# Kernel tuning notes

Measured on AMD Instinct MI355X. Metric: run time of the kernel, lower is better.

The kernel has to match this reference:

```python
import jax, jax.numpy as jnp
import numpy as np

D_MODEL = 1024
NUM_HEADS = 16
D_FF = 4096
EPS = 1e-5


def _linear(x, w, b):
    # torch nn.Linear: y = x @ W^T + b, W is [out, in]
    return jnp.einsum('bld,od->blo', x, w) + b


def _layer_norm(x, g, b):
    mu = jnp.mean(x, axis=-1, keepdims=True)
    var = jnp.mean(jnp.square(x - mu), axis=-1, keepdims=True)
    return (x - mu) / jnp.sqrt(var + EPS) * g + b


def _mha(q, k, v, wq, bq, wk, bk, wv, bv, wo, bo, mask, num_heads):
    B, Lq, D = q.shape
    hd = D // num_heads
    Q = _linear(q, wq, bq).reshape(B, Lq, num_heads, hd).transpose(0, 2, 1, 3)
    K = _linear(k, wk, bk).reshape(B, -1, num_heads, hd).transpose(0, 2, 1, 3)
    V = _linear(v, wv, bv).reshape(B, -1, num_heads, hd).transpose(0, 2, 1, 3)
    scale = jnp.sqrt(jnp.asarray(hd, dtype=q.dtype))
    energy = jnp.einsum('bhqd,bhkd->bhqk', Q, K) / scale  # [B,H,Lq,Lk]
    energy = jnp.where(mask, energy, jnp.asarray(-1e10, dtype=q.dtype))
    attn = jax.nn.softmax(energy, axis=-1)
    x = jnp.einsum('bhqk,bhkd->bhqd', attn, V)
    x = x.transpose(0, 2, 1, 3).reshape(B, Lq, D)
    return _linear(x, wo, bo), attn


def setup_inputs() -> dict:
    key = jax.random.key(0)
    ks = iter(jax.random.split(key, 40))
    B, T, S, D, F = 4, 1024, 1024, D_MODEL, D_FF
    inp = {
        'tgt': jax.random.normal(next(ks), (B, T, D), dtype=jnp.float32),
        'enc_src': jax.random.normal(next(ks), (B, S, D), dtype=jnp.float32),
        'tgt_mask': jnp.tril(jnp.ones((1, 1, T, T), dtype=bool)),
        'src_mask': jnp.ones((1, 1, 1, S), dtype=bool),
    }
    def lin(kk, o, i):
        return jax.random.normal(kk, (o, i), dtype=jnp.float32) * 0.02
    for pfx in ('sa', 'ca'):  # self-attn and cross-attn params
        for nm in ('q', 'k', 'v', 'o'):
            inp[f'{pfx}_w{nm}'] = lin(next(ks), D, D)
            inp[f'{pfx}_b{nm}'] = jnp.zeros((D,), dtype=jnp.float32)
    inp['ff_w1'] = lin(next(ks), F, D)
    inp['ff_b1'] = jnp.zeros((F,), dtype=jnp.float32)
    inp['ff_w2'] = lin(next(ks), D, F)
    inp['ff_b2'] = jnp.zeros((D,), dtype=jnp.float32)
    for i in (1, 2, 3):
        inp[f'ln{i}_g'] = jnp.ones((D,), dtype=jnp.float32)
        inp[f'ln{i}_b'] = jnp.zeros((D,), dtype=jnp.float32)
    return inp


def reference(tgt, enc_src, tgt_mask, src_mask,
              sa_wq, sa_bq, sa_wk, sa_bk, sa_wv, sa_bv, sa_wo, sa_bo,
              ca_wq, ca_bq, ca_wk, ca_bk, ca_wv, ca_bv, ca_wo, ca_bo,
              ff_w1, ff_b1, ff_w2, ff_b2,
              ln1_g, ln1_b, ln2_g, ln2_b, ln3_g, ln3_b):
    # dropout in eval mode (identity)
    _t, _ = _mha(tgt, tgt, tgt, sa_wq, sa_bq, sa_wk, sa_bk, sa_wv, sa_bv,
                 sa_wo, sa_bo, tgt_mask, NUM_HEADS)
    tgt = _layer_norm(tgt + _t, ln1_g, ln1_b)
    _t, attention = _mha(tgt, enc_src, enc_src, ca_wq, ca_bq, ca_wk, ca_bk,
                         ca_wv, ca_bv, ca_wo, ca_bo, src_mask, NUM_HEADS)
    tgt = _layer_norm(tgt + _t, ln2_g, ln2_b)
    _t = _linear(jax.nn.relu(_linear(tgt, ff_w1, ff_b1)), ff_w2, ff_b2)
    tgt = _layer_norm(tgt + _t, ln3_g, ln3_b)
    return tgt, attention
```

## Files before the change

### kernel.cpp

```cpp
#include <hip/hip_runtime.h>
#include <hip/hip_bf16.h>

#define BBATCH 4
#define TT 1024
#define SS 1024
#define DD 1024
#define HH 16
#define HD 64
#define FFD 4096
#define MM (BBATCH*TT)

using f32x4  = __attribute__((ext_vector_type(4))) float;
using s16x8  = __attribute__((ext_vector_type(8))) short;
using bf16x8 = __attribute__((ext_vector_type(8))) __bf16;

__device__ __forceinline__ unsigned short f2b(float f) {
  union { float f; unsigned int u; } x{f};
  unsigned int r = x.u + 0x7FFFu + ((x.u >> 16) & 1u);
  return (unsigned short)(r >> 16);
}

__device__ __forceinline__ float b2f(unsigned short u) {
  union { unsigned int i; float f; } x; x.i = (unsigned int)u << 16; return x.f;
}

__device__ __forceinline__ void gload16(const void* g, void* l) {
  __builtin_amdgcn_global_load_lds(
      (const __attribute__((address_space(1))) void*)g,
      (__attribute__((address_space(3))) void*)l, 16, 0, 0);
}

__device__ __forceinline__ f32x4 mfma_bf16(s16x8 a, s16x8 b, f32x4 c) {
  return __builtin_amdgcn_mfma_f32_16x16x32_bf16(
      __builtin_bit_cast(bf16x8, a), __builtin_bit_cast(bf16x8, b), c, 0, 0, 0);
}

__device__ __forceinline__ void xcd_swz(int gx, int& bn, int& bm) {
  int flat = blockIdx.y * gx + blockIdx.x;
  int nwg = gx * gridDim.y;
  int swz = (flat & 7) * (nwg >> 3) + (flat >> 3);
  bn = swz % gx; bm = swz / gx;
}

template <int JT>
__device__ __forceinline__ void stage_ab(
    const unsigned short* __restrict__ Ab, int lda,
    const unsigned short* __restrict__ Bb, int ldb,
    int kk, unsigned short* As, unsigned short* Bs, int r0, int c0, int wave)
{
#pragma unroll
  for (int s = 0; s < 2; s++) {
    int k2 = kk + s * 32;
    gload16(Ab + (size_t)r0 * lda + k2 + c0, As + s * 4096 + wave * 512);
    gload16(Ab + (size_t)(r0 + 64) * lda + k2 + c0, As + s * 4096 + wave * 512 + 2048);
    gload16(Bb + (size_t)r0 * ldb + k2 + c0, Bs + s * (JT * 1024) + wave * 512);
    if (JT == 4)
      gload16(Bb + (size_t)(r0 + 64) * ldb + k2 + c0, Bs + s * (JT * 1024) + wave * 512 + 2048);
  }
}

template <int JT>
__device__ __forceinline__ void gemm_core_db(
    const unsigned short* __restrict__ Ab, int lda,
    const unsigned short* __restrict__ Bb, int ldb,
    int K, unsigned short* As, unsigned short* Bs, f32x4 (&acc)[4][JT])
{
  const int tid = threadIdx.x, wave = tid >> 6, lane = tid & 63;
  const int r0 = tid >> 2, c0 = (tid & 3) * 8;
  const int wrow = (wave >> 1) * 64, wcol = (wave & 1) * 16 * JT;
  const int q = lane >> 4, rl = lane & 15;

  stage_ab<JT>(Ab, lda, Bb, ldb, 0, As, Bs, r0, c0, wave);
  const int nt = K >> 6;
  for (int t = 0; t < nt; t++) {
    __syncthreads();
    if (t + 1 < nt)
      stage_ab<JT>(Ab, lda, Bb, ldb, (t + 1) << 6,
                   As + ((t + 1) & 1) * 8192, Bs + ((t + 1) & 1) * (JT * 2048),
                   r0, c0, wave);
    const s16x8* Av = (const s16x8*)(As + (t & 1) * 8192);
    const s16x8* Bv = (const s16x8*)(Bs + (t & 1) * (JT * 2048));
#pragma unroll
    for (int s = 0; s < 2; s++) {
      s16x8 af[4], bfr[JT];
#pragma unroll
      for (int u = 0; u < 4; u++) af[u] = Av[s * 512 + (wrow + u * 16 + rl) * 4 + q];
#pragma unroll
      for (int u = 0; u < JT; u++) bfr[u] = Bv[s * (JT * 128) + (wcol + u * 16 + rl) * 4 + q];
#pragma unroll
      for (int i = 0; i < 4; i++)
#pragma unroll
        for (int j = 0; j < JT; j++)
          acc[i][j] = mfma_bf16(af[i], bfr[j], acc[i][j]);
    }
  }
}

template <int EPI, int JT>
__global__ __launch_bounds__(256) void gemm_bt(
    const unsigned short* __restrict__ A, int lda,
    const unsigned short* __restrict__ B, int ldb,
    const float* __restrict__ bias, const float* __restrict__ res,
    float* __restrict__ Cf, unsigned short* __restrict__ Cb, int ldc, int K)
{
  __shared__ __align__(16) unsigned short As[2 * 8192];
  __shared__ __align__(16) unsigned short Bs[2 * JT * 2048];
  int bm, bn;
  xcd_swz(gridDim.x, bn, bm);
  const int lane = threadIdx.x & 63, wave = threadIdx.x >> 6;
  const int wrow = (wave >> 1) * 64, wcol = (wave & 1) * 16 * JT;
  const int q = lane >> 4, rl = lane & 15;

  f32x4 acc[4][JT];
  f32x4 z = {0.f, 0.f, 0.f, 0.f};
#pragma unroll
  for (int i = 0; i < 4; i++)
#pragma unroll
    for (int j = 0; j < JT; j++) acc[i][j] = z;

  gemm_core_db<JT>(A + (size_t)bm * 128 * lda, lda,
                   B + (size_t)bn * (32 * JT) * ldb, ldb, K, As, Bs, acc);

#pragma unroll
  for (int i = 0; i < 4; i++) {
    int gm0 = bm * 128 + wrow + i * 16 + q * 4;
#pragma unroll
    for (int j = 0; j < JT; j++) {
      int gn = bn * (32 * JT) + wcol + j * 16 + rl;
      float bv = bias[gn];
#pragma unroll
      for (int r = 0; r < 4; r++) {
        size_t off = (size_t)(gm0 + r) * ldc + gn;
        float v = acc[i][j][r];
        if constexpr (EPI == 0) Cb[off] = f2b(v + bv);
        else if constexpr (EPI == 2) Cf[off] = v + bv + res[off];
        else Cb[off] = f2b(fmaxf(v + bv, 0.f));
      }
    }
  }
}

__global__ __launch_bounds__(256) void gemm_qkvkv(
    const unsigned short* __restrict__ Xb, const unsigned short* __restrict__ Eb,
    const unsigned short* __restrict__ Wqkv1, const unsigned short* __restrict__ Wkv2,
    const float* __restrict__ bqkv, const float* __restrict__ bkv,
    unsigned short* __restrict__ QKVb, unsigned short* __restrict__ KVb,
    unsigned short* __restrict__ Vt1, unsigned short* __restrict__ Vt2)
{
  __shared__ __align__(16) unsigned short lds[32768];
  unsigned short* As = lds;
  unsigned short* Bs = lds + 16384;
  const int tid = threadIdx.x;
  int bm, bn;
  xcd_swz(gridDim.x, bn, bm);
  const int lane = tid & 63, wave = tid >> 6;
  const int wrow = (wave >> 1) * 64, wcol = (wave & 1) * 64;
  const int q = lane >> 4, rl = lane & 15;

  const unsigned short *A, *Bw;
  const float* bias;
  unsigned short *C, *Vt;
  int ldc, vbn;
  bool isV;
  if (bn < 24) {
    A = Xb; Bw = Wqkv1 + (size_t)bn * 128 * 1024; bias = bqkv + bn * 128;
    C = QKVb + bn * 128; ldc = 3072;
    isV = (bn >= 16); Vt = Vt1; vbn = bn - 16;
  } else {
    int b2 = bn - 24;
    A = Eb; Bw = Wkv2 + (size_t)b2 * 128 * 1024; bias = bkv + b2 * 128;
    C = KVb + b2 * 128; ldc = 2048;
    isV = (b2 >= 8); Vt = Vt2; vbn = b2 - 8;
  }

  f32x4 acc[4][4];
  f32x4 z = {0.f, 0.f, 0.f, 0.f};
#pragma unroll
  for (int i = 0; i < 4; i++)
#pragma unroll
    for (int j = 0; j < 4; j++) acc[i][j] = z;

  gemm_core_db<4>(A + (size_t)bm * 128 * 1024, 1024, Bw, 1024, 1024, As, Bs, acc);

  if (!isV) {
#pragma unroll
    for (int i = 0; i < 4; i++) {
      int lr0 = wrow + i * 16 + q * 4;
#pragma unroll
      for (int j = 0; j < 4; j++) {
        int lc = wcol + j * 16 + rl;
        float bv = bias[lc];
#pragma unroll
        for (int r = 0; r < 4; r++)
          C[(size_t)(bm * 128 + lr0 + r) * ldc + lc] = f2b(acc[i][j][r] + bv);
      }
    }
  } else {
    __syncthreads();
#pragma unroll
    for (int i = 0; i < 4; i++) {
      int lr0 = wrow + i * 16 + q * 4;
#pragma unroll
      for (int j = 0; j < 4; j++) {
        int lc = wcol + j * 16 + rl;
        float bv = bias[lc];
        int base = lc * 128, sw = (lc & 7) << 2;
#pragma unroll
        for (int r = 0; r < 4; r++)
          lds[base + ((lr0 + r) ^ sw)] = f2b(acc[i][j][r] + bv);
      }
    }
    __syncthreads();
    const int b = bm >> 3, s0 = (bm & 7) * 128;
#pragma unroll
    for (int it = 0; it < 16; it++) {
      int idx = it * 256 + tid;
      int lc = idx >> 5, qa = idx & 31;
      ushort4 v4 = *(const ushort4*)&lds[lc * 128 + ((qa ^ (lc & 7)) << 2)];
      int h = vbn * 2 + (lc >> 6), d = lc & 63;
      *(ushort4*)&Vt[(((size_t)b * 16 + h) * 64 + d) * 1024 + s0 + qa * 4] = v4;
    }
  }
}

__device__ __forceinline__ void stage_k(
    const unsigned short* src, int ldk, unsigned short* Kbuf,
    int r0, int c0, int wave)
{
#pragma unroll
  for (int kq = 0; kq < 2; kq++) {
    gload16(src + (size_t)r0 * ldk + kq * 32 + c0, Kbuf + kq * 4096 + wave * 512);
    gload16(src + (size_t)(r0 + 64) * ldk + kq * 32 + c0, Kbuf + kq * 4096 + wave * 512 + 2048);
  }
}

__device__ __forceinline__ void sblock_qk(
    const unsigned short* Qs, const unsigned short* Ks,
    int wrow, int wcol, int q, int rl, f32x4 (&acc)[4][4])
{
  const s16x8* Qv = (const s16x8*)Qs;
  const s16x8* Kv = (const s16x8*)Ks;
  f32x4 z = {0.f, 0.f, 0.f, 0.f};
#pragma unroll
  for (int i = 0; i < 4; i++)
#pragma unroll
    for (int j = 0; j < 4; j++) acc[i][j] = z;
#pragma unroll
  for (int kq = 0; kq < 2; kq++) {
    s16x8 af[4], bf[4];
#pragma unroll
    for (int t = 0; t < 4; t++) af[t] = Qv[kq * 512 + (wrow + t * 16 + rl) * 4 + q];
#pragma unroll
    for (int t = 0; t < 4; t++) bf[t] = Kv[kq * 512 + (wcol + t * 16 + rl) * 4 + q];
#pragma unroll
    for (int i = 0; i < 4; i++)
#pragma unroll
      for (int j = 0; j < 4; j++)
        acc[i][j] = mfma_bf16(af[i], bf[j], acc[i][j]);
  }
}

__device__ __forceinline__ void load_vf(
    const unsigned short* Vbase, int c, int wc2, int q, int rl, s16x8 (&vf)[4][2])
{
#pragma unroll
  for (int ks = 0; ks < 4; ks++)
#pragma unroll
    for (int t = 0; t < 2; t++)
      vf[ks][t] = *(const s16x8*)(Vbase + (size_t)(wc2 + t * 16 + rl) * SS +
                                  c * 128 + ks * 32 + q * 8);
}

__device__ __forceinline__ void store_ps_swz(
    unsigned short* Ps, const f32x4 (&acc)[4][4], int wrow, int wcol, int q, int rl)
{
#pragma unroll
  for (int i = 0; i < 4; i++)
#pragma unroll
    for (int j = 0; j < 4; j++) {
      int col = wcol + j * 16 + rl;
      int ks = col >> 5, cc = col & 31;
#pragma unroll
      for (int r = 0; r < 4; r++) {
        int row = wrow + i * 16 + q * 4 + r;
        int unit = (row * 4 + (cc >> 3)) ^ ((row >> 1) & 3);
        Ps[ks * 4096 + unit * 8 + (cc & 7)] = f2b(acc[i][j][r]);
      }
    }
}

__device__ __forceinline__ void pv_swz(
    const unsigned short* Ps, const s16x8 (&vf)[4][2],
    int wrow, int q, int rl, f32x4 (&oacc)[4][2])
{
  const s16x8* Pv = (const s16x8*)Ps;
#pragma unroll
  for (int ks = 0; ks < 4; ks++) {
    s16x8 af[4];
#pragma unroll
    for (int t = 0; t < 4; t++) {
      int row = wrow + t * 16 + rl;
      af[t] = Pv[ks * 512 + ((row * 4 + q) ^ ((row >> 1) & 3))];
    }
#pragma unroll
    for (int i = 0; i < 4; i++)
#pragma unroll
      for (int jt = 0; jt < 2; jt++)
        oacc[i][jt] = mfma_bf16(af[i], vf[ks][jt], oacc[i][jt]);
  }
}

__global__ __launch_bounds__(256, 2) void flash_sa(
    const unsigned short* __restrict__ Qg, int ldq,
    const unsigned short* __restrict__ Kg, int ldk,
    const unsigned short* __restrict__ Vt,
    unsigned short* __restrict__ Og)
{
  __shared__ __align__(16) unsigned short Qs[2 * 128 * 32];
  __shared__ __align__(16) unsigned short Ks[2][2 * 128 * 32];
  __shared__ __align__(16) unsigned short Ps[4 * 128 * 32];

  const int tid = threadIdx.x, wave = tid >> 6, lane = tid & 63;
  const int q = lane >> 4, rl = lane & 15;
  const int bh = blockIdx.y, b = bh >> 4, h = bh & 15;
  const int bm = (bh & 32) ? (7 - blockIdx.x) : blockIdx.x;
  const int wrow = (wave >> 1) * 64, wcol = (wave & 1) * 64;
  const int wc2 = (wave & 1) * 32;
  const int r0 = tid >> 2, c0 = (tid & 3) * 8;

  const unsigned short* Qbase = Qg + ((size_t)b * TT + bm * 128) * ldq + h * HD;
  const unsigned short* Kbase = Kg + (size_t)b * SS * ldk + h * HD;
  const unsigned short* Vbase = Vt + ((size_t)bh << 16);

#pragma unroll
  for (int kq = 0; kq < 2; kq++) {
    gload16(Qbase + (size_t)r0 * ldq + kq * 32 + c0, Qs + kq * 4096 + wave * 512);
    gload16(Qbase + (size_t)(r0 + 64) * ldq + kq * 32 + c0, Qs + kq * 4096 + wave * 512 + 2048);
  }
  stage_k(Kbase, ldk, Ks[0], r0, c0, wave);
  const int nch = bm + 1;

  float l_run[4][4];
  f32x4 oacc[4][2];
  f32x4 z = {0.f, 0.f, 0.f, 0.f};
#pragma unroll
  for (int i = 0; i < 4; i++) {
    oacc[i][0] = z; oacc[i][1] = z;
#pragma unroll
    for (int r = 0; r < 4; r++) l_run[i][r] = 0.f;
  }

  for (int c = 0; c < nch; c++) {
    __syncthreads();
    if (c + 1 < nch)
      stage_k(Kbase + (size_t)(c + 1) * 128 * ldk, ldk, Ks[(c + 1) & 1], r0, c0, wave);
    s16x8 vf[4][2];
    load_vf(Vbase, c, wc2, q, rl, vf);
    f32x4 acc[4][4];
    sblock_qk(Qs, Ks[c & 1], wrow, wcol, q, rl, acc);
#pragma unroll
    for (int i = 0; i < 4; i++)
#pragma unroll
      for (int r = 0; r < 4; r++) {
#pragma unroll
        for (int j = 0; j < 4; j++) {
          float v = acc[i][j][r] * 0.125f;
          bool msk = (c == bm) && (wcol + j * 16 + rl) > (wrow + i * 16 + q * 4 + r);
          acc[i][j][r] = msk ? 0.f : __expf(v);
        }
        float s = acc[i][0][r] + acc[i][1][r] + acc[i][2][r] + acc[i][3][r];
#pragma unroll
        for (int off = 1; off < 16; off <<= 1) s += __shfl_xor(s, off);
        l_run[i][r] += s;
      }
    store_ps_swz(Ps, acc, wrow, wcol, q, rl);
    __syncthreads();
    pv_swz(Ps, vf, wrow, q, rl, oacc);
  }
  __syncthreads();

  float* red = (float*)Ps;
  if (rl == 0) {
#pragma unroll
    for (int i = 0; i < 4; i++)
#pragma unroll
      for (int r = 0; r < 4; r++)
        red[(wave & 1) * 128 + wrow + i * 16 + q * 4 + r] = l_run[i][r];
  }
  __syncthreads();

#pragma unroll
  for (int i = 0; i < 4; i++) {
#pragma unroll
    for (int r = 0; r < 4; r++) {
      int row = wrow + i * 16 + q * 4 + r;
      float inv = 1.0f / (red[row] + red[128 + row]);
      int grow = bm * 128 + row;
#pragma unroll
      for (int jt = 0; jt < 2; jt++) {
        int col = h * HD + wc2 + jt * 16 + rl;
        Og[((size_t)b * TT + grow) * DD + col] = f2b(oacc[i][jt][r] * inv);
      }
    }
  }
}

__global__ __launch_bounds__(256, 2) void flash_ca(
    const unsigned short* __restrict__ Qg, int ldq,
    const unsigned short* __restrict__ Kg, int ldk,
    const unsigned short* __restrict__ Vt,
    float* __restrict__ Pout,
    unsigned short* __restrict__ Og)
{
  __shared__ __align__(16) unsigned short Qs[2 * 128 * 32];
  __shared__ __align__(16) unsigned short Ks[2][2 * 128 * 32];
  __shared__ __align__(16) unsigned short Ps[4 * 128 * 32];

  const int tid = threadIdx.x, wave = tid >> 6, lane = tid & 63;
  const int q = lane >> 4, rl = lane & 15;
  const int bm = blockIdx.x, bh = blockIdx.y, b = bh >> 4, h = bh & 15;
  const int wrow = (wave >> 1) * 64, wcol = (wave & 1) * 64;
  const int wc2 = (wave & 1) * 32;
  const int r0 = tid >> 2, c0 = (tid & 3) * 8;

  const unsigned short* Qbase = Qg + ((size_t)b * TT + bm * 128) * ldq + h * HD;
  const unsigned short* Kbase = Kg + (size_t)b * SS * ldk + h * HD;
  const unsigned short* Vbase = Vt + ((size_t)bh << 16);

#pragma unroll
  for (int kq = 0; kq < 2; kq++) {
    gload16(Qbase + (size_t)r0 * ldq + kq * 32 + c0, Qs + kq * 4096 + wave * 512);
    gload16(Qbase + (size_t)(r0 + 64) * ldq + kq * 32 + c0, Qs + kq * 4096 + wave * 512 + 2048);
  }
  stage_k(Kbase, ldk, Ks[0], r0, c0, wave);

  float l_run[4][4];
#pragma unroll
  for (int i = 0; i < 4; i++)
#pragma unroll
    for (int r = 0; r < 4; r++) l_run[i][r] = 0.f;

  for (int c = 0; c < 8; c++) {
    __syncthreads();
    if (c < 7)
      stage_k(Kbase + (size_t)(c + 1) * 128 * ldk, ldk, Ks[(c + 1) & 1], r0, c0, wave);
    f32x4 acc[4][4];
    sblock_qk(Qs, Ks[c & 1], wrow, wcol, q, rl, acc);
#pragma unroll
    for (int i = 0; i < 4; i++)
#pragma unroll
      for (int r = 0; r < 4; r++) {
        float s = __expf(acc[i][0][r] * 0.125f) + __expf(acc[i][1][r] * 0.125f) +
                  __expf(acc[i][2][r] * 0.125f) + __expf(acc[i][3][r] * 0.125f);
#pragma unroll
        for (int off = 1; off < 16; off <<= 1) s += __shfl_xor(s, off);
        l_run[i][r] += s;
      }
  }
  float* red = (float*)Ps;
  if (rl == 0) {
#pragma unroll
    for (int i = 0; i < 4; i++)
#pragma unroll
      for (int r = 0; r < 4; r++)
        red[(wave & 1) * 128 + wrow + i * 16 + q * 4 + r] = l_run[i][r];
  }
  __syncthreads();
  float invl[4][4];
#pragma unroll
  for (int i = 0; i < 4; i++)
#pragma unroll
    for (int r = 0; r < 4; r++) {
      int row = wrow + i * 16 + q * 4 + r;
      invl[i][r] = 1.0f / (red[row] + red[128 + row]);
    }

  f32x4 oacc[4][2];
  f32x4 z = {0.f, 0.f, 0.f, 0.f};
#pragma unroll
  for (int i = 0; i < 4; i++) { oacc[i][0] = z; oacc[i][1] = z; }
  stage_k(Kbase, ldk, Ks[0], r0, c0, wave);

  for (int c = 0; c < 8; c++) {
    __syncthreads();
    if (c < 7)
      stage_k(Kbase + (size_t)(c + 1) * 128 * ldk, ldk, Ks[(c + 1) & 1], r0, c0, wave);
    s16x8 vf[4][2];
    load_vf(Vbase, c, wc2, q, rl, vf);
    f32x4 acc[4][4];
    sblock_qk(Qs, Ks[c & 1], wrow, wcol, q, rl, acc);
#pragma unroll
    for (int i = 0; i < 4; i++)
#pragma unroll
      for (int j = 0; j < 4; j++)
#pragma unroll
        for (int r = 0; r < 4; r++)
          acc[i][j][r] = __expf(acc[i][j][r] * 0.125f) * invl[i][r];
    store_ps_swz(Ps, acc, wrow, wcol, q, rl);
    __syncthreads();
#pragma unroll
    for (int it = 0; it < 8; it++) {
      int idx = it * 256 + tid;
      int ks = idx >> 9, rw = (idx >> 2) & 127, u = idx & 3;
      s16x8 pv = ((const s16x8*)Ps)[ks * 512 + ((rw * 4 + u) ^ ((rw >> 1) & 3))];
      float4 lo = make_float4(b2f((unsigned short)pv[0]), b2f((unsigned short)pv[1]),
                              b2f((unsigned short)pv[2]), b2f((unsigned short)pv[3]));
      float4 hi = make_float4(b2f((unsigned short)pv[4]), b2f((unsigned short)pv[5]),
                              b2f((unsigned short)pv[6]), b2f((unsigned short)pv[7]));
      float* dst = Pout + ((size_t)bh << 20) + ((size_t)(bm * 128 + rw) << 10) +
                   c * 128 + ks * 32 + u * 8;
      ((float4*)dst)[0] = lo;
      ((float4*)dst)[1] = hi;
    }
    pv_swz(Ps, vf, wrow, q, rl, oacc);
  }

#pragma unroll
  for (int i = 0; i < 4; i++)
#pragma unroll
    for (int jt = 0; jt < 2; jt++)
#pragma unroll
      for (int r = 0; r < 4; r++) {
        int row = bm * 128 + wrow + i * 16 + q * 4 + r;
        int col = h * HD + wc2 + jt * 16 + rl;
        Og[((size_t)b * TT + row) * DD + col] = f2b(oacc[i][jt][r]);
      }
}

__global__ __launch_bounds__(256) void ln_k(
    const float* __restrict__ src, const float* __restrict__ g,
    const float* __restrict__ b, float* __restrict__ dstf,
    unsigned short* __restrict__ dstb)
{
  __shared__ float sh[10];
  const size_t row = blockIdx.x;
  const int tid = threadIdx.x;
  float4 v = ((const float4*)(src + (row << 10)))[tid];
  float s = v.x + v.y + v.z + v.w;
  float ss = v.x * v.x + v.y * v.y + v.z * v.z + v.w * v.w;
  for (int o = 32; o; o >>= 1) { s += __shfl_down(s, o); ss += __shfl_down(ss, o); }
  if ((tid & 63) == 0) { sh[tid >> 6] = s; sh[4 + (tid >> 6)] = ss; }
  __syncthreads();
  if (tid == 0) {
    sh[8] = sh[0] + sh[1] + sh[2] + sh[3];
    sh[9] = sh[4] + sh[5] + sh[6] + sh[7];
  }
  __syncthreads();
  const float mean = sh[8] * (1.0f / DD);
  const float var = sh[9] * (1.0f / DD) - mean * mean;
  const float inv = rsqrtf(var + 1e-5f);
  float4 gv = ((const float4*)g)[tid];
  float4 bv = ((const float4*)b)[tid];
  float4 y;
  y.x = (v.x - mean) * inv * gv.x + bv.x;
  y.y = (v.y - mean) * inv * gv.y + bv.y;
  y.z = (v.z - mean) * inv * gv.z + bv.z;
  y.w = (v.w - mean) * inv * gv.w + bv.w;
  if (dstf) ((float4*)(dstf + (row << 10)))[tid] = y;
  if (dstb) {
    ushort4 o = make_ushort4(f2b(y.x), f2b(y.y), f2b(y.z), f2b(y.w));
    ((ushort4*)(dstb + (row << 10)))[tid] = o;
  }
}

struct CvtArgs {
  const float* src[12];
  unsigned short* dst[12];
  const float *bq, *bk, *bv, *bk2, *bv2;
  float *bqkv, *bkv;
};

__global__ __launch_bounds__(256) void cvt_all(CvtArgs a) {
  const int blk = blockIdx.x;
  if (blk >= 24576) {
    int i = (blk - 24576) * 256 + threadIdx.x;
    if (i < 1024) a.bqkv[i] = a.bq[i];
    else if (i < 2048) a.bqkv[i] = a.bk[i - 1024];
    else if (i < 3072) a.bqkv[i] = a.bv[i - 2048];
    else if (i < 4096) a.bkv[i - 3072] = a.bk2[i - 3072];
    else if (i < 5120) a.bkv[i - 3072] = a.bv2[i - 4096 + 1024];
    return;
  }
  constexpr int st[13] = {0,       1048576, 2097152, 2359296, 2621440,
                          2883584, 3145728, 3407872, 3670016, 3932160,
                          4194304, 5242880, 6291456};
  int i = blk * 256 + threadIdx.x;
  int s = 0;
#pragma unroll
  for (int k = 1; k < 12; k++) s += (i >= st[k]) ? 1 : 0;
  int j = i - st[s];
  float4 v = ((const float4*)a.src[s])[j];
  ushort4 o = make_ushort4(f2b(v.x), f2b(v.y), f2b(v.z), f2b(v.w));
  ((ushort4*)a.dst[s])[j] = o;
}


extern "C" void kernel_launch(void* const* d_in, const int* in_sizes, int n_in,
                              void* d_out, int out_size, void* d_ws, size_t ws_size,
                              hipStream_t stream)
{
  const float* tgt = (const float*)d_in[0];
  const float* enc = (const float*)d_in[1];
  const float* sa_wq = (const float*)d_in[4];  const float* sa_bq = (const float*)d_in[5];
  const float* sa_wk = (const float*)d_in[6];  const float* sa_bk = (const float*)d_in[7];
  const float* sa_wv = (const float*)d_in[8];  const float* sa_bv = (const float*)d_in[9];
  const float* sa_wo = (const float*)d_in[10]; const float* sa_bo = (const float*)d_in[11];
  const float* ca_wq = (const float*)d_in[12]; const float* ca_bq = (const float*)d_in[13];
  const float* ca_wk = (const float*)d_in[14]; const float* ca_bk = (const float*)d_in[15];
  const float* ca_wv = (const float*)d_in[16]; const float* ca_bv = (const float*)d_in[17];
  const float* ca_wo = (const float*)d_in[18]; const float* ca_bo = (const float*)d_in[19];
  const float* ff_w1 = (const float*)d_in[20]; const float* ff_b1 = (const float*)d_in[21];
  const float* ff_w2 = (const float*)d_in[22]; const float* ff_b2 = (const float*)d_in[23];
  const float* ln1_g = (const float*)d_in[24]; const float* ln1_b = (const float*)d_in[25];
  const float* ln2_g = (const float*)d_in[26]; const float* ln2_b = (const float*)d_in[27];
  const float* ln3_g = (const float*)d_in[28]; const float* ln3_b = (const float*)d_in[29];

  float* out_tgt = (float*)d_out;
  float* out_attn = (float*)d_out + (size_t)MM * DD;

  char* w = (char*)d_ws;
  size_t off = 0;
  auto alloc = [&](size_t bytes) { void* p = w + off; off += (bytes + 255) & ~(size_t)255; return p; };
  unsigned short* Xb   = (unsigned short*)alloc((size_t)MM * DD * 2);
  unsigned short* Eb   = (unsigned short*)alloc((size_t)MM * DD * 2);
  unsigned short* Wq1  = (unsigned short*)alloc((size_t)DD * DD * 2);
  unsigned short* Wk1  = (unsigned short*)alloc((size_t)DD * DD * 2);
  unsigned short* Wv1  = (unsigned short*)alloc((size_t)DD * DD * 2);
  unsigned short* Wo1  = (unsigned short*)alloc((size_t)DD * DD * 2);
  unsigned short* Wq2  = (unsigned short*)alloc((size_t)DD * DD * 2);
  unsigned short* Wk2  = (unsigned short*)alloc((size_t)DD * DD * 2);
  unsigned short* Wv2  = (unsigned short*)alloc((size_t)DD * DD * 2);
  unsigned short* Wo2  = (unsigned short*)alloc((size_t)DD * DD * 2);
  unsigned short* Wf1  = (unsigned short*)alloc((size_t)FFD * DD * 2);
  unsigned short* Wf2  = (unsigned short*)alloc((size_t)DD * FFD * 2);
  unsigned short* QKVb = (unsigned short*)alloc((size_t)MM * 3 * DD * 2);
  unsigned short* KVb  = (unsigned short*)alloc((size_t)MM * 2 * DD * 2);
  unsigned short* Qca  = (unsigned short*)alloc((size_t)MM * DD * 2);
  unsigned short* Vt1  = (unsigned short*)alloc((size_t)MM * DD * 2);
  unsigned short* Vt2  = (unsigned short*)alloc((size_t)MM * DD * 2);
  unsigned short* Ob   = (unsigned short*)alloc((size_t)MM * DD * 2);
  float*          res1 = (float*)alloc((size_t)MM * DD * 4);
  unsigned short* t1b  = (unsigned short*)alloc((size_t)MM * DD * 2);
  float*          res2 = (float*)alloc((size_t)MM * DD * 4);
  unsigned short* t2b  = (unsigned short*)alloc((size_t)MM * DD * 2);
  unsigned short* Fb   = (unsigned short*)alloc((size_t)MM * FFD * 2);
  float*          bqkv = (float*)alloc(3072 * 4);
  float*          bkv  = (float*)alloc(2048 * 4);

  CvtArgs ca;
  ca.src[0] = tgt;   ca.dst[0] = Xb;
  ca.src[1] = enc;   ca.dst[1] = Eb;
  ca.src[2] = sa_wq; ca.dst[2] = Wq1;
  ca.src[3] = sa_wk; ca.dst[3] = Wk1;
  ca.src[4] = sa_wv; ca.dst[4] = Wv1;
  ca.src[5] = sa_wo; ca.dst[5] = Wo1;
  ca.src[6] = ca_wq; ca.dst[6] = Wq2;
  ca.src[7] = ca_wk; ca.dst[7] = Wk2;
  ca.src[8] = ca_wv; ca.dst[8] = Wv2;
  ca.src[9] = ca_wo; ca.dst[9] = Wo2;
  ca.src[10] = ff_w1; ca.dst[10] = Wf1;
  ca.src[11] = ff_w2; ca.dst[11] = Wf2;
  ca.bq = sa_bq; ca.bk = sa_bk; ca.bv = sa_bv; ca.bk2 = ca_bk; ca.bv2 = ca_bv;
  ca.bqkv = bqkv; ca.bkv = bkv;

  cvt_all<<<24596, 256, 0, stream>>>(ca);

  const dim3 gPRJ(40, 32);
  const dim3 gN64(16, 32);
  const dim3 gFF1(32, 32);
  const dim3 gFl(8, 64);

  gemm_qkvkv<<<gPRJ, 256, 0, stream>>>(Xb, Eb, Wq1, Wk2, bqkv, bkv,
                                       QKVb, KVb, Vt1, Vt2);

  flash_sa<<<gFl, 256, 0, stream>>>(QKVb, 3 * DD, QKVb + DD, 3 * DD, Vt1, Ob);
  gemm_bt<2, 2><<<gN64, 256, 0, stream>>>(Ob, DD, Wo1, DD, sa_bo, tgt, res1, nullptr, DD, DD);
  ln_k<<<MM, 256, 0, stream>>>(res1, ln1_g, ln1_b, res1, t1b);

  gemm_bt<0, 2><<<gN64, 256, 0, stream>>>(t1b, DD, Wq2, DD, ca_bq, nullptr, nullptr, Qca, DD, DD);
  flash_ca<<<gFl, 256, 0, stream>>>(Qca, DD, KVb, 2 * DD, Vt2, out_attn, Ob);
  gemm_bt<2, 2><<<gN64, 256, 0, stream>>>(Ob, DD, Wo2, DD, ca_bo, res1, res2, nullptr, DD, DD);
  ln_k<<<MM, 256, 0, stream>>>(res2, ln2_g, ln2_b, res2, t2b);

  gemm_bt<3, 4><<<gFF1, 256, 0, stream>>>(t2b, DD, Wf1, DD, ff_b1, nullptr, nullptr, Fb, FFD, DD);
  gemm_bt<2, 2><<<gN64, 256, 0, stream>>>(Fb, FFD, Wf2, FFD, ff_b2, res2, res1, nullptr, DD, FFD);
  ln_k<<<MM, 256, 0, stream>>>(res1, ln3_g, ln3_b, out_tgt, nullptr);
}
```

Baseline: 762.6 us.

## Load GEMM B operand directly into registers, bypassing LDS staging

The GEMM cores stop staging the weight (B) tile through shared memory. Each wave now loads its own B fragments straight from global memory into double-buffered registers one K-step ahead, and only A stays in LDS. This cuts LDS footprint and LDS read traffic, which may allow higher occupancy. In exchange it raises register pressure, and B rows are no longer shared between the two wave-rows, so the same B data is fetched twice from global/L2 with a less coalesced pattern.

```diff
diff --git a/kernel.cpp b/kernel.cpp
--- a/kernel.cpp
+++ b/kernel.cpp
@@ -42,57 +42,52 @@
   bn = swz % gx; bm = swz / gx;
 }
 
+__device__ __forceinline__ void stage_a(
+    const unsigned short* __restrict__ Ab, int lda, int kk,
+    unsigned short* As, int r0, int c0, int wave)
+{
+#pragma unroll
+  for (int s = 0; s < 2; s++) {
+    gload16(Ab + (size_t)r0 * lda + kk + s * 32 + c0, As + s * 4096 + wave * 512);
+    gload16(Ab + (size_t)(r0 + 64) * lda + kk + s * 32 + c0, As + s * 4096 + wave * 512 + 2048);
+  }
+}
+
 template <int JT>
-__device__ __forceinline__ void stage_ab(
+__device__ __forceinline__ void load_breg(
+    const unsigned short* __restrict__ Bl, int ldb, int kk, s16x8 (&br)[2][JT])
+{
+#pragma unroll
+  for (int s = 0; s < 2; s++)
+#pragma unroll
+    for (int u = 0; u < JT; u++)
+      br[s][u] = *(const s16x8*)(Bl + (size_t)u * 16 * ldb + kk + s * 32);
+}
+
+template <int JT>
+__device__ __forceinline__ void gemm_step(
     const unsigned short* __restrict__ Ab, int lda,
-    const unsigned short* __restrict__ Bb, int ldb,
-    int kk, unsigned short* As, unsigned short* Bs, int r0, int c0, int wave)
-{
+    const unsigned short* __restrict__ Bl, int ldb,
+    int t, int nt, unsigned short* AsCur, unsigned short* AsNext,
+    s16x8 (&brCur)[2][JT], s16x8 (&brNext)[2][JT],
+    f32x4 (&acc)[4][JT], int r0, int c0, int wave, int wrow, int q, int rl)
+{
+  __syncthreads();
+  if (t + 1 < nt) {
+    stage_a(Ab, lda, (t + 1) << 6, AsNext, r0, c0, wave);
+    load_breg<JT>(Bl, ldb, (t + 1) << 6, brNext);
+  }
+  const s16x8* Av = (const s16x8*)AsCur;
 #pragma unroll
   for (int s = 0; s < 2; s++) {
-    int k2 = kk + s * 32;
-    gload16(Ab + (size_t)r0 * lda + k2 + c0, As + s * 4096 + wave * 512);
-    gload16(Ab + (size_t)(r0 + 64) * lda + k2 + c0, As + s * 4096 + wave * 512 + 2048);
-    gload16(Bb + (size_t)r0 * ldb + k2 + c0, Bs + s * (JT * 1024) + wave * 512);
-    if (JT == 4)
-      gload16(Bb + (size_t)(r0 + 64) * ldb + k2 + c0, Bs + s * (JT * 1024) + wave * 512 + 2048);
-  }
-}
-
-template <int JT>
-__device__ __forceinline__ void gemm_core_db(
-    const unsigned short* __restrict__ Ab, int lda,
-    const unsigned short* __restrict__ Bb, int ldb,
-    int K, unsigned short* As, unsigned short* Bs, f32x4 (&acc)[4][JT])
-{
-  const int tid = threadIdx.x, wave = tid >> 6, lane = tid & 63;
-  const int r0 = tid >> 2, c0 = (tid & 3) * 8;
-  const int wrow = (wave >> 1) * 64, wcol = (wave & 1) * 16 * JT;
-  const int q = lane >> 4, rl = lane & 15;
-
-  stage_ab<JT>(Ab, lda, Bb, ldb, 0, As, Bs, r0, c0, wave);
-  const int nt = K >> 6;
-  for (int t = 0; t < nt; t++) {
-    __syncthreads();
-    if (t + 1 < nt)
-      stage_ab<JT>(Ab, lda, Bb, ldb, (t + 1) << 6,
-                   As + ((t + 1) & 1) * 8192, Bs + ((t + 1) & 1) * (JT * 2048),
-                   r0, c0, wave);
-    const s16x8* Av = (const s16x8*)(As + (t & 1) * 8192);
-    const s16x8* Bv = (const s16x8*)(Bs + (t & 1) * (JT * 2048));
-#pragma unroll
-    for (int s = 0; s < 2; s++) {
-      s16x8 af[4], bfr[JT];
-#pragma unroll
-      for (int u = 0; u < 4; u++) af[u] = Av[s * 512 + (wrow + u * 16 + rl) * 4 + q];
-#pragma unroll
-      for (int u = 0; u < JT; u++) bfr[u] = Bv[s * (JT * 128) + (wcol + u * 16 + rl) * 4 + q];
-#pragma unroll
-      for (int i = 0; i < 4; i++)
-#pragma unroll
-        for (int j = 0; j < JT; j++)
-          acc[i][j] = mfma_bf16(af[i], bfr[j], acc[i][j]);
-    }
+    s16x8 af[4];
+#pragma unroll
+    for (int u = 0; u < 4; u++) af[u] = Av[s * 512 + (wrow + u * 16 + rl) * 4 + q];
+#pragma unroll
+    for (int i = 0; i < 4; i++)
+#pragma unroll
+      for (int j = 0; j < JT; j++)
+        acc[i][j] = mfma_bf16(af[i], brCur[s][j], acc[i][j]);
   }
 }
 
@@ -104,12 +99,16 @@
     float* __restrict__ Cf, unsigned short* __restrict__ Cb, int ldc, int K)
 {
   __shared__ __align__(16) unsigned short As[2 * 8192];
-  __shared__ __align__(16) unsigned short Bs[2 * JT * 2048];
   int bm, bn;
   xcd_swz(gridDim.x, bn, bm);
-  const int lane = threadIdx.x & 63, wave = threadIdx.x >> 6;
+  const int tid = threadIdx.x;
+  const int lane = tid & 63, wave = tid >> 6;
   const int wrow = (wave >> 1) * 64, wcol = (wave & 1) * 16 * JT;
   const int q = lane >> 4, rl = lane & 15;
+  const int r0 = tid >> 2, c0 = (tid & 3) * 8;
+
+  const unsigned short* Ab = A + (size_t)bm * 128 * lda;
+  const unsigned short* Bl = B + (size_t)(bn * (32 * JT) + wcol + rl) * ldb + q * 8;
 
   f32x4 acc[4][JT];
   f32x4 z = {0.f, 0.f, 0.f, 0.f};
@@ -118,8 +117,16 @@
 #pragma unroll
     for (int j = 0; j < JT; j++) acc[i][j] = z;
 
-  gemm_core_db<JT>(A + (size_t)bm * 128 * lda, lda,
-                   B + (size_t)bn * (32 * JT) * ldb, ldb, K, As, Bs, acc);
+  s16x8 br0[2][JT], br1[2][JT];
+  stage_a(Ab, lda, 0, As, r0, c0, wave);
+  load_breg<JT>(Bl, ldb, 0, br0);
+  const int nt = K >> 6;
+  for (int t = 0; t < nt; t += 2) {
+    gemm_step<JT>(Ab, lda, Bl, ldb, t, nt, As, As + 8192, br0, br1,
+                  acc, r0, c0, wave, wrow, q, rl);
+    gemm_step<JT>(Ab, lda, Bl, ldb, t + 1, nt, As + 8192, As, br1, br0,
+                  acc, r0, c0, wave, wrow, q, rl);
+  }
 
 #pragma unroll
   for (int i = 0; i < 4; i++) {
@@ -147,15 +154,14 @@
     unsigned short* __restrict__ QKVb, unsigned short* __restrict__ KVb,
     unsigned short* __restrict__ Vt1, unsigned short* __restrict__ Vt2)
 {
-  __shared__ __align__(16) unsigned short lds[32768];
-  unsigned short* As = lds;
-  unsigned short* Bs = lds + 16384;
+  __shared__ __align__(16) unsigned short lds[2 * 8192];
   const int tid = threadIdx.x;
   int bm, bn;
   xcd_swz(gridDim.x, bn, bm);
   const int lane = tid & 63, wave = tid >> 6;
   const int wrow = (wave >> 1) * 64, wcol = (wave & 1) * 64;
   const int q = lane >> 4, rl = lane & 15;
+  const int r0 = tid >> 2, c0 = (tid & 3) * 8;
 
   const unsigned short *A, *Bw;
   const float* bias;
@@ -172,6 +178,8 @@
     C = KVb + b2 * 128; ldc = 2048;
     isV = (b2 >= 8); Vt = Vt2; vbn = b2 - 8;
   }
+  const unsigned short* Ab = A + (size_t)bm * 128 * 1024;
+  const unsigned short* Bl = Bw + (size_t)(wcol + rl) * 1024 + q * 8;
 
   f32x4 acc[4][4];
   f32x4 z = {0.f, 0.f, 0.f, 0.f};
@@ -180,7 +188,15 @@
 #pragma unroll
     for (int j = 0; j < 4; j++) acc[i][j] = z;
 
-  gemm_core_db<4>(A + (size_t)bm * 128 * 1024, 1024, Bw, 1024, 1024, As, Bs, acc);
+  s16x8 br0[2][4], br1[2][4];
+  stage_a(Ab, 1024, 0, lds, r0, c0, wave);
+  load_breg<4>(Bl, 1024, 0, br0);
+  for (int t = 0; t < 16; t += 2) {
+    gemm_step<4>(Ab, 1024, Bl, 1024, t, 16, lds, lds + 8192, br0, br1,
+                 acc, r0, c0, wave, wrow, q, rl);
+    gemm_step<4>(Ab, 1024, Bl, 1024, t + 1, 16, lds + 8192, lds, br1, br0,
+                 acc, r0, c0, wave, wrow, q, rl);
+  }
 
   if (!isV) {
 #pragma unroll
```

Result: slower. 856.9 us (+12.4%).
